# Kernel optimization log

Hardware: AMD Instinct MI355X
Metric: run time of the kernel (lower is better)

## Reference

```python
import jax, jax.numpy as jnp
import numpy as np

D, K, B, IMG, NCH = 128, 512, 8, 128, 3


def adder2d(x, w, k, stride, pad):
    # AdderNet L1 'convolution': y[b,co,l] = -sum_p |patch[b,p,l] - w[co,p]|
    # x: [B,C,H,W], w: [Cout, C*k*k]
    p = jax.lax.conv_general_dilated_patches(x, (k, k), (stride, stride), [(pad, pad), (pad, pad)])
    Bb, P, Ho, Wo = p.shape
    p = p.reshape(Bb, P, Ho * Wo)  # [B, C*k*k, L]
    def one(wc):  # wc: [P] -> [B, L]; sequential over Cout to bound memory
        return -jnp.sum(jnp.abs(p - wc[None, :, None]), axis=1)
    o = jax.lax.map(one, w)  # [Cout, B, L]
    return jnp.transpose(o, (1, 0, 2)).reshape(Bb, w.shape[0], Ho, Wo)


def bn(x, g, b, eps=1e-5):
    # eval-mode BatchNorm2d with running_mean=0, running_var=1
    s = g * jax.lax.rsqrt(jnp.asarray(1.0 + eps, x.dtype))
    return x * s[None, :, None, None] + b[None, :, None, None]


def conv2d(x, w, b, pad):
    y = jax.lax.conv_general_dilated(x, w, (1, 1), [(pad, pad), (pad, pad)],
                                     dimension_numbers=('NCHW', 'OIHW', 'NCHW'))
    return y + b[None, :, None, None]


def up2x(x):  # nn.Upsample(scale_factor=2, bilinear, align_corners=False)
    Bb, C, H, W = x.shape
    return jax.image.resize(x, (Bb, C, 2 * H, 2 * W), method='bilinear')


def adder_resblock(x, w1, w2, g, b):
    # [ReLU, adder3x3, BN, ReLU, adder1x1] + residual
    h = jax.nn.relu(x)
    h = adder2d(h, w1, 3, 1, 1)
    h = bn(h, g, b)
    h = jax.nn.relu(h)
    h = adder2d(h, w2, 1, 1, 0)
    return x + h


def conv_resblock(x, w1, b1, w2, b2):
    # [ReLU, conv3x3, ReLU, conv1x1] + residual (bn=False in decoder)
    h = jax.nn.relu(x)
    h = conv2d(h, w1, b1, 1)
    h = jax.nn.relu(h)
    h = conv2d(h, w2, b2, 0)
    return x + h


def vq_forward(z_e, E):
    # NearestEmbed: E is [d, k]
    Bb, C, H, W = z_e.shape
    flat = jnp.transpose(z_e, (0, 2, 3, 1)).reshape(-1, C)  # [N, d]
    d2 = (jnp.sum(flat * flat, axis=1, keepdims=True)
          - 2.0 * (flat @ E) + jnp.sum(E * E, axis=0)[None, :])  # [N, k]
    argmin = jnp.argmin(d2, axis=1)  # [N]
    q = jnp.take(E.T, argmin, axis=0)  # [N, d]
    # weight_sg=True path: straight-through to z_e, no grad to E
    zq_flat = flat + jax.lax.stop_gradient(q - flat)
    z_q = jnp.transpose(zq_flat.reshape(Bb, H, W, C), (0, 3, 1, 2))
    # emb path: z_e detached, grad flows to E through the gather
    emb = jnp.transpose(q.reshape(Bb, H, W, C), (0, 3, 1, 2))
    return z_q, emb, argmin.reshape(Bb, H, W)


def reference(x, we1, we2, ae1_w1, ae1_w2, ae2_w1, ae2_w2, bn_gamma, bn_beta,
              emb_weight, rd1_w1, rd1_b1, rd1_w2, rd1_b2, rd2_w1, rd2_b1,
              rd2_w2, rd2_b2, cd1_w, cd1_b, cd2_w, cd2_b):
    g, b = bn_gamma, bn_beta
    h = adder2d(x, we1, 4, 2, 1)
    h = jax.nn.relu(bn(h, g[0], b[0]))
    h = adder2d(h, we2, 4, 2, 1)
    h = jax.nn.relu(bn(h, g[1], b[1]))
    h = adder_resblock(h, ae1_w1, ae1_w2, g[2], b[2])
    h = bn(h, g[3], b[3])
    h = adder_resblock(h, ae2_w1, ae2_w2, g[4], b[4])
    z_e = bn(h, g[5], b[5])  # bne4 (gamma = 1/40)

    z_q, emb, argmin = vq_forward(z_e, emb_weight)

    y = conv_resblock(z_q, rd1_w1, rd1_b1, rd1_w2, rd1_b2)
    y = bn(y, g[6], b[6])
    y = conv_resblock(y, rd2_w1, rd2_b1, rd2_w2, rd2_b2)
    y = up2x(y)
    y = conv2d(y, cd1_w, cd1_b, 1)
    y = jax.nn.relu(bn(y, g[7], b[7]))
    y = up2x(y)
    y = conv2d(y, cd2_w, cd2_b, 1)
    y = jnp.tanh(y)
    return (y, z_e, emb, argmin)


def setup_inputs() -> dict:
    key = jax.random.key(0)
    ks = jax.random.split(key, 16)
    f = lambda k, shp: (0.02 * jax.random.normal(k, shp)).astype(jnp.float32)
    inp = {}
    inp['x'] = jax.random.normal(ks[0], (B, NCH, IMG, IMG), jnp.float32)
    inp['we1'] = f(ks[1], (D, NCH * 16))       # adder 4x4 s2
    inp['we2'] = f(ks[2], (D, D * 16))
    inp['ae1_w1'] = f(ks[3], (D, D * 9))       # adder 3x3
    inp['ae1_w2'] = f(ks[4], (D, D))           # adder 1x1
    inp['ae2_w1'] = f(ks[5], (D, D * 9))
    inp['ae2_w2'] = f(ks[6], (D, D))
    inp['bn_gamma'] = jnp.ones((8, D), jnp.float32).at[5].set(1.0 / 40.0)
    inp['bn_beta'] = jnp.zeros((8, D), jnp.float32)
    inp['emb_weight'] = f(ks[7], (D, K))
    inp['rd1_w1'] = f(ks[8], (D, D, 3, 3)); inp['rd1_b1'] = jnp.zeros(D, jnp.float32)
    inp['rd1_w2'] = f(ks[9], (D, D, 1, 1)); inp['rd1_b2'] = jnp.zeros(D, jnp.float32)
    inp['rd2_w1'] = f(ks[10], (D, D, 3, 3)); inp['rd2_b1'] = jnp.zeros(D, jnp.float32)
    inp['rd2_w2'] = f(ks[11], (D, D, 1, 1)); inp['rd2_b2'] = jnp.zeros(D, jnp.float32)
    inp['cd1_w'] = f(ks[12], (D, D, 3, 3)); inp['cd1_b'] = jnp.zeros(D, jnp.float32)
    inp['cd2_w'] = f(ks[13], (NCH, D, 3, 3)); inp['cd2_b'] = jnp.zeros(NCH, jnp.float32)
    return inp
```

## Files before the change

### kernel.cpp

```cpp
#include <hip/hip_runtime.h>
#include <math.h>

constexpr int Dc = 128;
constexpr int Kc = 512;
constexpr int Bc = 8;

template<int ISADD, int K, int STRIDE, int PAD, int IT, int EPI, int CIN, int CH,
         int PW, int OUT_ROWS, int WOUT, int WIN, int HIN, int HOUT, int COBW,
         int NW, int KSPLIT>
__global__ __launch_bounds__(NW * 64)
void lds_layer(const float* __restrict__ x, const float* __restrict__ w,
               const float* __restrict__ bias,
               const float* __restrict__ itG, const float* __restrict__ itB,
               const float* __restrict__ res,
               const float* __restrict__ rG, const float* __restrict__ rB,
               const float* __restrict__ oG, const float* __restrict__ oB,
               float* __restrict__ out) {
  constexpr int BT = NW * 64;
  constexpr int NWG = NW / KSPLIT;
  constexpr int CINW = CIN / KSPLIT;
  constexpr int CHS = KSPLIT * CH;
  constexpr int KK = K * K;
  constexpr int SPAN = (PW - 1) * STRIDE + K;
  constexpr int IN_ROWS = (OUT_ROWS - 1) * STRIDE + K;
  constexpr int WPAD = (WOUT - 1) * STRIDE + K;
  constexpr int WLDS = (WPAD + 3) & ~3;
  constexpr int PGW = WOUT / PW;
  static_assert(OUT_ROWS * PGW == 64, "one wave covers the pixel tile");
  static_assert(NW % KSPLIT == 0 && CIN % KSPLIT == 0 && CINW % CH == 0, "split");
  static_assert(KSPLIT == 1 ||
                NWG * 64 * PW * COBW <= CHS * IN_ROWS * WLDS, "scratch fits");
  constexpr int NBAND = HOUT / OUT_ROWS;
  constexpr int W4 = WIN / 4;
  constexpr int NELEM4 = CHS * IN_ROWS * W4;
  constexpr int NIT4 = (NELEM4 + BT - 1) / BT;
  constexpr bool EXACT = (NELEM4 % BT) == 0;
  const float r15 = rsqrtf(1.0f + 1e-5f);

  __shared__ alignas(16) float lds[CHS][IN_ROWS][WLDS];

  int tid = threadIdx.x;
  int gb = blockIdx.x;
  int cg = gb / (Bc * NBAND);
  int rem = gb % (Bc * NBAND);
  int band = rem % NBAND;
  int b = rem / NBAND;
  int wv = __builtin_amdgcn_readfirstlane(tid >> 6);
  int lane = tid & 63;
  int grp = wv / NWG;
  int wloc = wv % NWG;
  int co0 = cg * (NWG * COBW) + wloc * COBW;
  int pr = lane / PGW, pc = lane % PGW;
  int oh = band * OUT_ROWS + pr;
  int ow0 = pc * PW;
  int yi0 = band * OUT_ROWS * STRIDE - PAD;

  for (int e = tid; e < CHS * IN_ROWS * WLDS; e += BT) ((float*)lds)[e] = 0.f;

  float acc[PW][COBW];
#pragma unroll
  for (int p = 0; p < PW; ++p)
#pragma unroll
    for (int j = 0; j < COBW; ++j)
      acc[p][j] = (ISADD || grp != 0) ? 0.f : bias[co0 + j];

  const float* xb = x + (long)b * CIN * HIN * WIN;
  float4 rbuf[NIT4];

  auto stage = [&](int cc) {
#pragma unroll
    for (int it = 0; it < NIT4; ++it) {
      int e = it * BT + tid;
      if (!EXACT && e >= NELEM4) break;
      int c4 = e % W4;
      int r = (e / W4) % IN_ROWS;
      int ch2 = e / (W4 * IN_ROWS);
      int gc = cc + (ch2 % CH) + (ch2 / CH) * CINW;
      int yi = yi0 + r;
      float4 v = make_float4(0.f, 0.f, 0.f, 0.f);
      if (yi >= 0 && yi < HIN) {
        v = *(const float4*)&xb[((long)gc * HIN + yi) * WIN + 4 * c4];
        if (IT == 1) {
          v.x = fmaxf(v.x, 0.f); v.y = fmaxf(v.y, 0.f);
          v.z = fmaxf(v.z, 0.f); v.w = fmaxf(v.w, 0.f);
        }
        if (IT == 2) {
          float sc = itG[gc] * r15, bc = itB[gc];
          v.x = fmaxf(fmaf(v.x, sc, bc), 0.f);
          v.y = fmaxf(fmaf(v.y, sc, bc), 0.f);
          v.z = fmaxf(fmaf(v.z, sc, bc), 0.f);
          v.w = fmaxf(fmaf(v.w, sc, bc), 0.f);
        }
      }
      rbuf[it] = v;
    }
  };
  auto towrite = [&]() {
#pragma unroll
    for (int it = 0; it < NIT4; ++it) {
      int e = it * BT + tid;
      if (!EXACT && e >= NELEM4) break;
      int c4 = e % W4;
      int r = (e / W4) % IN_ROWS;
      int ch2 = e / (W4 * IN_ROWS);
      float* p = &lds[ch2][r][4 * c4 + PAD];
      float4 v = rbuf[it];
      p[0] = v.x; p[1] = v.y; p[2] = v.z; p[3] = v.w;
    }
  };

  stage(0);
  for (int cc = 0; cc < CINW; cc += CH) {
    __syncthreads();
    towrite();
    __syncthreads();
    if (cc + CH < CINW) stage(cc + CH);
#pragma unroll 2
    for (int chl = 0; chl < CH; ++chl) {
      float vbuf[K][SPAN];
#pragma unroll
      for (int kh = 0; kh < K; ++kh) {
        const float* rp0 = &lds[grp * CH + chl][pr * STRIDE + kh][ow0 * STRIDE];
        if constexpr (SPAN == 6 && (PW * STRIDE) % 4 == 0) {
          float4 a = *(const float4*)rp0;
          float2 c2 = *(const float2*)(rp0 + 4);
          vbuf[kh][0] = a.x; vbuf[kh][1] = a.y; vbuf[kh][2] = a.z;
          vbuf[kh][3] = a.w; vbuf[kh][4] = c2.x; vbuf[kh][5] = c2.y;
        } else if constexpr (SPAN == 4 && (PW * STRIDE) % 2 == 0) {
          float2 a = *(const float2*)rp0;
          float2 c2 = *(const float2*)(rp0 + 2);
          vbuf[kh][0] = a.x; vbuf[kh][1] = a.y;
          vbuf[kh][2] = c2.x; vbuf[kh][3] = c2.y;
        } else if constexpr (SPAN == 2 && (PW * STRIDE) % 2 == 0) {
          float2 a = *(const float2*)rp0;
          vbuf[kh][0] = a.x; vbuf[kh][1] = a.y;
        } else {
#pragma unroll
          for (int s = 0; s < SPAN; ++s) vbuf[kh][s] = rp0[s];
        }
      }
      const float* wc = w + ((long)co0 * CIN + (grp * CINW + cc + chl)) * KK;
#pragma unroll
      for (int kh = 0; kh < K; ++kh)
#pragma unroll
        for (int kw = 0; kw < K; ++kw)
#pragma unroll
          for (int j = 0; j < COBW; ++j) {
            float ww = wc[(long)j * CIN * KK + kh * K + kw];
#pragma unroll
            for (int p = 0; p < PW; ++p) {
              float v = vbuf[kh][p * STRIDE + kw];
              if (ISADD) acc[p][j] += fabsf(v - ww);
              else       acc[p][j] = fmaf(v, ww, acc[p][j]);
            }
          }
    }
  }

  if constexpr (KSPLIT >= 2) {
    float* scr = (float*)lds;
    int sb = (wloc * 64 + lane) * (PW * COBW);
#pragma unroll
    for (int g = 1; g < KSPLIT; ++g) {
      __syncthreads();
      if (grp == g) {
#pragma unroll
        for (int p = 0; p < PW; ++p)
#pragma unroll
          for (int j = 0; j < COBW; ++j) scr[sb + p * COBW + j] = acc[p][j];
      }
      __syncthreads();
      if (grp == 0) {
#pragma unroll
        for (int p = 0; p < PW; ++p)
#pragma unroll
          for (int j = 0; j < COBW; ++j) acc[p][j] += scr[sb + p * COBW + j];
      }
    }
    if (grp != 0) return;
  }

  long obase = ((long)(b * Dc + co0) * HOUT + oh) * WOUT + ow0;
  float* ob = out + obase;
  const float* rp = (EPI == 2 || EPI == 3 || EPI == 6) ? res + obase : nullptr;
  constexpr long hw = (long)HOUT * WOUT;
#pragma unroll
  for (int j = 0; j < COBW; ++j) {
    float og = 0.f, obb = 0.f, rg = 0.f, rbb = 0.f;
    if (EPI == 1 || EPI == 6) { og = oG[co0 + j] * r15; obb = oB[co0 + j]; }
    if (EPI == 3 || EPI == 6) { rg = rG[co0 + j] * r15; rbb = rB[co0 + j]; }
#pragma unroll
    for (int p = 0; p < PW; ++p) {
      float val = ISADD ? -acc[p][j] : acc[p][j];
      if (EPI == 1) val = fmaxf(fmaf(val, og, obb), 0.f);
      if (EPI == 2) val = rp[j * hw + p] + val;
      if (EPI == 3) val = fmaf(rp[j * hw + p], rg, rbb) + val;
      if (EPI == 5) val = fmaxf(val, 0.f);
      if (EPI == 6) val = fmaf(fmaf(rp[j * hw + p], rg, rbb) + val, og, obb);
      ob[j * hw + p] = val;
    }
  }
}

template<int ISADD, int EPI, int COBW>
__global__ __launch_bounds__(256)
void pw1x1(const float* __restrict__ x, const float* __restrict__ w,
           const float* __restrict__ bias,
           const float* __restrict__ res,
           const float* __restrict__ rG, const float* __restrict__ rB,
           const float* __restrict__ oG, const float* __restrict__ oB,
           float* __restrict__ out) {
  constexpr int HW = 1024;
  constexpr int CIN = Dc;
  constexpr int KS = 4;
  constexpr int CSEG = CIN / KS;
  constexpr int PXB = 128;
  constexpr int NPG = HW / PXB;
  constexpr int OPT = (PXB * COBW) / 256;
  static_assert(OPT * 256 == PXB * COBW, "combine exact");
  const float r15 = rsqrtf(1.0f + 1e-5f);

  __shared__ float scr[KS][COBW][PXB];

  int tid = threadIdx.x;
  int wv = __builtin_amdgcn_readfirstlane(tid >> 6);
  int lane = tid & 63;
  int gb = blockIdx.x;
  int cg = gb / (Bc * NPG);
  int rem = gb % (Bc * NPG);
  int pg = rem % NPG;
  int b = rem / NPG;
  int co0 = cg * COBW;
  int px = pg * PXB + lane * 2;

  const float* xc = x + ((long)b * CIN + wv * CSEG) * HW + px;
  const float* wseg = w + wv * CSEG;

  float acc[2][COBW];
#pragma unroll
  for (int p = 0; p < 2; ++p)
#pragma unroll
    for (int j = 0; j < COBW; ++j) acc[p][j] = 0.f;

#pragma unroll 4
  for (int c = 0; c < CSEG; ++c) {
    float2 v = *(const float2*)&xc[(long)c * HW];
#pragma unroll
    for (int j = 0; j < COBW; ++j) {
      float ww = wseg[(long)(co0 + j) * CIN + c];
      if (ISADD) {
        acc[0][j] += fabsf(v.x - ww);
        acc[1][j] += fabsf(v.y - ww);
      } else {
        acc[0][j] = fmaf(v.x, ww, acc[0][j]);
        acc[1][j] = fmaf(v.y, ww, acc[1][j]);
      }
    }
  }

#pragma unroll
  for (int j = 0; j < COBW; ++j) {
    float2 t = make_float2(acc[0][j], acc[1][j]);
    *(float2*)&scr[wv][j][lane * 2] = t;
  }
  __syncthreads();

#pragma unroll
  for (int k = 0; k < OPT; ++k) {
    int e = k * 256 + tid;
    int pxl = e % PXB;
    int j = e / PXB;
    float s = scr[0][j][pxl] + scr[1][j][pxl] + scr[2][j][pxl] + scr[3][j][pxl];
    float val = ISADD ? -s : s + bias[co0 + j];
    long oidx = ((long)b * Dc + co0 + j) * HW + pg * PXB + pxl;
    if (EPI == 2) val = res[oidx] + val;
    if (EPI == 3) {
      float rg = rG[co0 + j] * r15, rbb = rB[co0 + j];
      val = fmaf(res[oidx], rg, rbb) + val;
    }
    if (EPI == 6) {
      float rg = rG[co0 + j] * r15, rbb = rB[co0 + j];
      float og = oG[co0 + j] * r15, obb = oB[co0 + j];
      val = fmaf(fmaf(res[oidx], rg, rbb) + val, og, obb);
    }
    out[oidx] = val;
  }
}

__device__ __forceinline__ void up_coef(int p, int H, int& i0, int& i1, float& w0, float& w1) {
  int m = p >> 1;
  if ((p & 1) == 0) { i0 = (m > 0) ? m - 1 : 0; i1 = m; w0 = 0.25f; w1 = 0.75f; }
  else              { i0 = m; i1 = (m + 1 < H) ? m + 1 : H - 1; w0 = 0.75f; w1 = 0.25f; }
}

__global__ void up2x_kernel(const float* __restrict__ in, float* __restrict__ out,
                            int C, int H, int W) {
  int H2 = 2 * H, W2 = 2 * W;
  int i = blockIdx.x * blockDim.x + threadIdx.x;
  int total = Bc * C * H2 * W2;
  if (i >= total) return;
  int ow = i % W2; int t = i / W2;
  int oh = t % H2; t /= H2;
  int c = t % C; int b = t / C;
  int y0, y1, x0, x1; float wy0, wy1, wx0, wx1;
  up_coef(oh, H, y0, y1, wy0, wy1);
  up_coef(ow, W, x0, x1, wx0, wx1);
  const float* p = in + (b * C + c) * H * W;
  float v = wy0 * (wx0 * p[y0 * W + x0] + wx1 * p[y0 * W + x1])
          + wy1 * (wx0 * p[y1 * W + x0] + wx1 * p[y1 * W + x1]);
  out[i] = v;
}

__global__ __launch_bounds__(256)
void conv3x3_up_tanh_ks(const float* __restrict__ x, const float* __restrict__ w,
                        const float* __restrict__ bias, float* __restrict__ out,
                        int Hs, int Ws, int Cout) {
  constexpr int CIN = Dc;
  constexpr int SEG = 4;
  constexpr int CSEG = CIN / SEG;
  constexpr int QB = 64;
  __shared__ float scr[SEG][4][QB];

  int H2 = 2 * Hs, W2 = 2 * Ws;
  int nq = Hs * Ws;
  int tid = threadIdx.x;
  int q_l = tid % QB;
  int seg = tid / QB;
  int gq = blockIdx.x * QB + q_l;
  int q = gq % nq; int t2 = gq / nq;
  int co = t2 % Cout; int b = t2 / Cout;
  int n = q % Ws, m = q / Ws;
  int rows[3] = { (m > 0) ? m - 1 : 0, m, (m + 1 < Hs) ? m + 1 : Hs - 1 };
  int cols[3] = { (n > 0) ? n - 1 : 0, n, (n + 1 < Ws) ? n + 1 : Ws - 1 };
  float rv[4] = { (2 * m - 1 >= 0) ? 1.f : 0.f, 1.f, 1.f, (2 * m + 2 < H2) ? 1.f : 0.f };
  float cv[4] = { (2 * n - 1 >= 0) ? 1.f : 0.f, 1.f, 1.f, (2 * n + 2 < W2) ? 1.f : 0.f };
  float acc[4] = { 0.f, 0.f, 0.f, 0.f };
  const float* xb = x + (b * CIN + seg * CSEG) * nq;
  const float* wb = w + (co * CIN + seg * CSEG) * 9;
  for (int c = 0; c < CSEG; ++c) {
    const float* xc = xb + c * nq;
    float s[3][3];
#pragma unroll
    for (int a = 0; a < 3; ++a)
#pragma unroll
      for (int e = 0; e < 3; ++e) s[a][e] = xc[rows[a] * Ws + cols[e]];
    float rb[4][3];
#pragma unroll
    for (int e = 0; e < 3; ++e) {
      rb[0][e] = fmaf(0.75f, s[0][e], 0.25f * s[1][e]);
      rb[1][e] = fmaf(0.25f, s[0][e], 0.75f * s[1][e]);
      rb[2][e] = fmaf(0.75f, s[1][e], 0.25f * s[2][e]);
      rb[3][e] = fmaf(0.25f, s[1][e], 0.75f * s[2][e]);
    }
    float u[4][4];
#pragma unroll
    for (int di = 0; di < 4; ++di) {
      float rm = rv[di];
      u[di][0] = fmaf(0.75f, rb[di][0], 0.25f * rb[di][1]) * rm * cv[0];
      u[di][1] = fmaf(0.25f, rb[di][0], 0.75f * rb[di][1]) * rm * cv[1];
      u[di][2] = fmaf(0.75f, rb[di][1], 0.25f * rb[di][2]) * rm * cv[2];
      u[di][3] = fmaf(0.25f, rb[di][1], 0.75f * rb[di][2]) * rm * cv[3];
    }
    const float* wc = wb + c * 9;
#pragma unroll
    for (int kh = 0; kh < 3; ++kh)
#pragma unroll
      for (int kw = 0; kw < 3; ++kw) {
        float ww = wc[kh * 3 + kw];
        acc[0] = fmaf(u[kh][kw],         ww, acc[0]);
        acc[1] = fmaf(u[kh][kw + 1],     ww, acc[1]);
        acc[2] = fmaf(u[kh + 1][kw],     ww, acc[2]);
        acc[3] = fmaf(u[kh + 1][kw + 1], ww, acc[3]);
      }
  }
#pragma unroll
  for (int di = 0; di < 4; ++di) scr[seg][di][q_l] = acc[di];
  __syncthreads();
  int di = tid / QB;
  float sum = scr[0][di][q_l] + scr[1][di][q_l] + scr[2][di][q_l]
            + scr[3][di][q_l] + bias[co];
  out[(long)(b * Cout + co) * H2 * W2 + (2 * m + (di >> 1)) * W2 + 2 * n + (di & 1)]
      = tanhf(sum);
}

__global__ __launch_bounds__(256)
void vq_kernel8(const float* __restrict__ z_e, const float* __restrict__ E,
                float* __restrict__ emb, float* __restrict__ argmin_out) {
  constexpr int HW = 1024;
  __shared__ alignas(16) float f[8][Dc];
  __shared__ float d2s[8][256];
  __shared__ int   ks[8][256];
  int tid = threadIdx.x;
  int n0 = blockIdx.x * 8;
  int b = n0 >> 10;
  int rem = n0 & 1023;
  const float* zb = z_e + (long)b * Dc * HW + rem;
#pragma unroll
  for (int i = 0; i < 4; ++i) {
    int e = i * 256 + tid;
    int p = e & 7, d = e >> 3;
    f[p][d] = zb[d * HW + p];
  }
  __syncthreads();
  float f2 = 0.f;
  if (tid < 8) {
    for (int d = 0; d < Dc; ++d) f2 += f[tid][d] * f[tid][d];
    d2s[tid][0] = f2;
  }
  __syncthreads();
  float f2v[8];
#pragma unroll
  for (int p = 0; p < 8; ++p) f2v[p] = d2s[p][0];
  __syncthreads();

  float best[8]; int bk[8];
#pragma unroll
  for (int p = 0; p < 8; ++p) { best[p] = 3.4e38f; bk[p] = 0; }
  for (int kk = tid; kk < Kc; kk += 256) {
    float dot[8];
#pragma unroll
    for (int p = 0; p < 8; ++p) dot[p] = 0.f;
    float e2k = 0.f;
    for (int d4 = 0; d4 < Dc; d4 += 4) {
      float e0 = E[(long)(d4 + 0) * Kc + kk];
      float e1 = E[(long)(d4 + 1) * Kc + kk];
      float e2c = E[(long)(d4 + 2) * Kc + kk];
      float e3 = E[(long)(d4 + 3) * Kc + kk];
      e2k = fmaf(e0, e0, e2k);
      e2k = fmaf(e1, e1, e2k);
      e2k = fmaf(e2c, e2c, e2k);
      e2k = fmaf(e3, e3, e2k);
#pragma unroll
      for (int p = 0; p < 8; ++p) {
        float4 fv = *(const float4*)&f[p][d4];
        dot[p] = fmaf(fv.x, e0, dot[p]);
        dot[p] = fmaf(fv.y, e1, dot[p]);
        dot[p] = fmaf(fv.z, e2c, dot[p]);
        dot[p] = fmaf(fv.w, e3, dot[p]);
      }
    }
#pragma unroll
    for (int p = 0; p < 8; ++p) {
      float d2 = f2v[p] - 2.f * dot[p] + e2k;
      if (d2 < best[p] || (d2 == best[p] && kk < bk[p])) { best[p] = d2; bk[p] = kk; }
    }
  }
#pragma unroll
  for (int p = 0; p < 8; ++p) { d2s[p][tid] = best[p]; ks[p][tid] = bk[p]; }
  __syncthreads();
  for (int s = 128; s > 0; s >>= 1) {
    if (tid < s) {
#pragma unroll
      for (int p = 0; p < 8; ++p) {
        float ob = d2s[p][tid + s]; int ok = ks[p][tid + s];
        if (ob < d2s[p][tid] || (ob == d2s[p][tid] && ok < ks[p][tid])) {
          d2s[p][tid] = ob; ks[p][tid] = ok;
        }
      }
    }
    __syncthreads();
  }
  if (tid < 8) argmin_out[n0 + tid] = (float)ks[tid][0];
  float* eb = emb + (long)b * Dc * HW + rem;
#pragma unroll
  for (int i = 0; i < 4; ++i) {
    int e = i * 256 + tid;
    int p = e & 7, d = e >> 3;
    eb[d * HW + p] = E[d * Kc + ks[p][0]];
  }
}

extern "C" void kernel_launch(void* const* d_in, const int* in_sizes, int n_in,
                              void* d_out, int out_size, void* d_ws, size_t ws_size,
                              hipStream_t stream) {
  const float* x      = (const float*)d_in[0];
  const float* we1    = (const float*)d_in[1];
  const float* we2    = (const float*)d_in[2];
  const float* ae1_w1 = (const float*)d_in[3];
  const float* ae1_w2 = (const float*)d_in[4];
  const float* ae2_w1 = (const float*)d_in[5];
  const float* ae2_w2 = (const float*)d_in[6];
  const float* bn_g   = (const float*)d_in[7];
  const float* bn_b   = (const float*)d_in[8];
  const float* embw   = (const float*)d_in[9];
  const float* rd1_w1 = (const float*)d_in[10];
  const float* rd1_b1 = (const float*)d_in[11];
  const float* rd1_w2 = (const float*)d_in[12];
  const float* rd1_b2 = (const float*)d_in[13];
  const float* rd2_w1 = (const float*)d_in[14];
  const float* rd2_b1 = (const float*)d_in[15];
  const float* rd2_w2 = (const float*)d_in[16];
  const float* rd2_b2 = (const float*)d_in[17];
  const float* cd1_w  = (const float*)d_in[18];
  const float* cd1_b  = (const float*)d_in[19];
  const float* cd2_w  = (const float*)d_in[20];
  const float* cd2_b  = (const float*)d_in[21];

  const float* g0 = bn_g + 0 * Dc; const float* b0 = bn_b + 0 * Dc;
  const float* g1 = bn_g + 1 * Dc; const float* b1 = bn_b + 1 * Dc;
  const float* g2 = bn_g + 2 * Dc; const float* b2 = bn_b + 2 * Dc;
  const float* g3 = bn_g + 3 * Dc; const float* b3 = bn_b + 3 * Dc;
  const float* g4 = bn_g + 4 * Dc; const float* b4 = bn_b + 4 * Dc;
  const float* g5 = bn_g + 5 * Dc; const float* b5 = bn_b + 5 * Dc;
  const float* g6 = bn_g + 6 * Dc; const float* b6 = bn_b + 6 * Dc;
  const float* g7 = bn_g + 7 * Dc; const float* b7 = bn_b + 7 * Dc;

  float* W64a = (float*)d_ws;
  float* W64b = W64a + 4194304;
  float* Wa   = W64b + 4194304;
  float* Wb   = Wa + 1048576;
  float* Wc   = Wb + 1048576;

  float* out_y   = (float*)d_out;
  float* out_ze  = out_y  + 393216;
  float* out_emb = out_ze + 1048576;
  float* out_am  = out_emb + 1048576;

  const int TB = 256;
  const int TB8 = 512;
  auto nb = [](int n) { return (n + 255) / 256; };
  const int N64 = Bc * Dc * 64 * 64;
  const float* nul = nullptr;

  const int G32s = 16 * Bc * 8;
  const int Gwe1 = 8 * Bc * 32;
  const int Gcd1 = 4 * Bc * 32;
  const int Gpw  = 32 * Bc * 8;
  const int Gct  = Bc * 3 * 64 * 64 / 64;

  lds_layer<1,4,2,1, 0,1, 3,3, 2, 2,64,128,128,64, 4,4,1><<<Gwe1, TB, 0, stream>>>(
      x, we1, nul, nul, nul, nul, nul, nul, g0, b0, W64a);
  lds_layer<1,4,2,1, 0,1, Dc,4, 2, 4,32,64,64,32, 2,8,2><<<G32s, TB8, 0, stream>>>(
      W64a, we2, nul, nul, nul, nul, nul, nul, g1, b1, Wa);
  lds_layer<1,3,1,1, 0,1, Dc,16, 2, 4,32,32,32,32, 2,8,2><<<G32s, TB8, 0, stream>>>(
      Wa, ae1_w1, nul, nul, nul, nul, nul, nul, g2, b2, Wb);
  pw1x1<1,2,4><<<Gpw, TB, 0, stream>>>(
      Wb, ae1_w2, nul, Wa, nul, nul, nul, nul, Wc);
  lds_layer<1,3,1,1, 2,1, Dc,16, 2, 4,32,32,32,32, 2,8,2><<<G32s, TB8, 0, stream>>>(
      Wc, ae2_w1, nul, g3, b3, nul, nul, nul, g4, b4, Wb);
  pw1x1<1,6,4><<<Gpw, TB, 0, stream>>>(
      Wb, ae2_w2, nul, Wc, g3, b3, g5, b5, out_ze);

  vq_kernel8<<<Bc * 1024 / 8, 256, 0, stream>>>(out_ze, embw, out_emb, out_am);

  lds_layer<0,3,1,1, 1,5, Dc,16, 2, 4,32,32,32,32, 2,8,2><<<G32s, TB8, 0, stream>>>(
      out_emb, rd1_w1, rd1_b1, nul, nul, nul, nul, nul, nul, nul, Wb);
  pw1x1<0,2,4><<<Gpw, TB, 0, stream>>>(
      Wb, rd1_w2, rd1_b2, out_emb, nul, nul, nul, nul, Wa);
  lds_layer<0,3,1,1, 2,5, Dc,16, 2, 4,32,32,32,32, 2,8,2><<<G32s, TB8, 0, stream>>>(
      Wa, rd2_w1, rd2_b1, g6, b6, nul, nul, nul, nul, nul, Wb);
  pw1x1<0,3,4><<<Gpw, TB, 0, stream>>>(
      Wb, rd2_w2, rd2_b2, Wa, g6, b6, nul, nul, Wc);

  up2x_kernel<<<nb(N64), TB, 0, stream>>>(Wc, W64a, Dc, 32, 32);
  lds_layer<0,3,1,1, 0,1, Dc,8, 2, 2,64,64,64,64, 8,8,2><<<Gcd1, TB8, 0, stream>>>(
      W64a, cd1_w, cd1_b, nul, nul, nul, nul, nul, g7, b7, W64b);

  conv3x3_up_tanh_ks<<<Gct, TB, 0, stream>>>(W64b, cd2_w, cd2_b, out_y, 64, 64, 3);
}
```

Baseline: 783.7 us.

## Vectorize upsample to two outputs per thread, widen VQ and tanh-conv parallelism

The bilinear upsample kernel now has each thread compute two horizontally adjacent outputs from a shared three-column row blend and store them as a float2, which cuts redundant loads and index math. The VQ kernel moves to 512 threads so each thread handles exactly one codebook entry with no inner loop, and the argmin reduction gains one more level. The final upsample+conv+tanh kernel splits the channel reduction into 8 segments over 32 query points per block instead of 4 over 64, doubling the grid. These are three separate parallelism and vectorization tweaks to small kernels, each trading extra blocks or reduction steps for shorter per-thread work.

```diff
diff --git a/kernel.cpp b/kernel.cpp
--- a/kernel.cpp
+++ b/kernel.cpp
@@ -293,22 +293,25 @@
   else              { i0 = m; i1 = (m + 1 < H) ? m + 1 : H - 1; w0 = 0.75f; w1 = 0.25f; }
 }
 
-__global__ void up2x_kernel(const float* __restrict__ in, float* __restrict__ out,
-                            int C, int H, int W) {
+__global__ void up2x2_kernel(const float* __restrict__ in, float* __restrict__ out,
+                             int C, int H, int W) {
   int H2 = 2 * H, W2 = 2 * W;
   int i = blockIdx.x * blockDim.x + threadIdx.x;
-  int total = Bc * C * H2 * W2;
+  int total = Bc * C * H2 * W;
   if (i >= total) return;
-  int ow = i % W2; int t = i / W2;
-  int oh = t % H2; t /= H2;
-  int c = t % C; int b = t / C;
-  int y0, y1, x0, x1; float wy0, wy1, wx0, wx1;
+  int t = i % W; int u = i / W;
+  int oh = u % H2; u /= H2;
+  int c = u % C; int b = u / C;
+  int y0, y1; float wy0, wy1;
   up_coef(oh, H, y0, y1, wy0, wy1);
-  up_coef(ow, W, x0, x1, wx0, wx1);
   const float* p = in + (b * C + c) * H * W;
-  float v = wy0 * (wx0 * p[y0 * W + x0] + wx1 * p[y0 * W + x1])
-          + wy1 * (wx0 * p[y1 * W + x0] + wx1 * p[y1 * W + x1]);
-  out[i] = v;
+  int xm1 = (t > 0) ? t - 1 : 0;
+  int xp1 = (t + 1 < W) ? t + 1 : W - 1;
+  float r0 = wy0 * p[y0 * W + xm1] + wy1 * p[y1 * W + xm1];
+  float r1 = wy0 * p[y0 * W + t]   + wy1 * p[y1 * W + t];
+  float r2 = wy0 * p[y0 * W + xp1] + wy1 * p[y1 * W + xp1];
+  float2 o = make_float2(0.25f * r0 + 0.75f * r1, 0.75f * r1 + 0.25f * r2);
+  *(float2*)&out[((long)(b * C + c) * H2 + oh) * W2 + 2 * t] = o;
 }
 
 __global__ __launch_bounds__(256)
@@ -316,9 +319,9 @@
                         const float* __restrict__ bias, float* __restrict__ out,
                         int Hs, int Ws, int Cout) {
   constexpr int CIN = Dc;
-  constexpr int SEG = 4;
+  constexpr int SEG = 8;
   constexpr int CSEG = CIN / SEG;
-  constexpr int QB = 64;
+  constexpr int QB = 32;
   __shared__ float scr[SEG][4][QB];
 
   int H2 = 2 * Hs, W2 = 2 * Ws;
@@ -376,28 +379,36 @@
 #pragma unroll
   for (int di = 0; di < 4; ++di) scr[seg][di][q_l] = acc[di];
   __syncthreads();
-  int di = tid / QB;
-  float sum = scr[0][di][q_l] + scr[1][di][q_l] + scr[2][di][q_l]
-            + scr[3][di][q_l] + bias[co];
-  out[(long)(b * Cout + co) * H2 * W2 + (2 * m + (di >> 1)) * W2 + 2 * n + (di & 1)]
-      = tanhf(sum);
-}
-
-__global__ __launch_bounds__(256)
+  if (tid < 4 * QB) {
+    int ql2 = tid % QB;
+    int di = tid / QB;
+    int gq2 = blockIdx.x * QB + ql2;
+    int q2 = gq2 % nq; int t3 = gq2 / nq;
+    int co2 = t3 % Cout; int b2 = t3 / Cout;
+    int n2 = q2 % Ws, m2 = q2 / Ws;
+    float sum = bias[co2];
+#pragma unroll
+    for (int sg = 0; sg < SEG; ++sg) sum += scr[sg][di][ql2];
+    out[(long)(b2 * Cout + co2) * H2 * W2 + (2 * m2 + (di >> 1)) * W2 + 2 * n2 + (di & 1)]
+        = tanhf(sum);
+  }
+}
+
+__global__ __launch_bounds__(512)
 void vq_kernel8(const float* __restrict__ z_e, const float* __restrict__ E,
                 float* __restrict__ emb, float* __restrict__ argmin_out) {
   constexpr int HW = 1024;
   __shared__ alignas(16) float f[8][Dc];
-  __shared__ float d2s[8][256];
-  __shared__ int   ks[8][256];
+  __shared__ float d2s[8][512];
+  __shared__ int   ks[8][512];
   int tid = threadIdx.x;
   int n0 = blockIdx.x * 8;
   int b = n0 >> 10;
   int rem = n0 & 1023;
   const float* zb = z_e + (long)b * Dc * HW + rem;
 #pragma unroll
-  for (int i = 0; i < 4; ++i) {
-    int e = i * 256 + tid;
+  for (int i = 0; i < 2; ++i) {
+    int e = i * 512 + tid;
     int p = e & 7, d = e >> 3;
     f[p][d] = zb[d * HW + p];
   }
@@ -413,42 +424,36 @@
   for (int p = 0; p < 8; ++p) f2v[p] = d2s[p][0];
   __syncthreads();
 
-  float best[8]; int bk[8];
-#pragma unroll
-  for (int p = 0; p < 8; ++p) { best[p] = 3.4e38f; bk[p] = 0; }
-  for (int kk = tid; kk < Kc; kk += 256) {
-    float dot[8];
-#pragma unroll
-    for (int p = 0; p < 8; ++p) dot[p] = 0.f;
-    float e2k = 0.f;
-    for (int d4 = 0; d4 < Dc; d4 += 4) {
-      float e0 = E[(long)(d4 + 0) * Kc + kk];
-      float e1 = E[(long)(d4 + 1) * Kc + kk];
-      float e2c = E[(long)(d4 + 2) * Kc + kk];
-      float e3 = E[(long)(d4 + 3) * Kc + kk];
-      e2k = fmaf(e0, e0, e2k);
-      e2k = fmaf(e1, e1, e2k);
-      e2k = fmaf(e2c, e2c, e2k);
-      e2k = fmaf(e3, e3, e2k);
-#pragma unroll
-      for (int p = 0; p < 8; ++p) {
-        float4 fv = *(const float4*)&f[p][d4];
-        dot[p] = fmaf(fv.x, e0, dot[p]);
-        dot[p] = fmaf(fv.y, e1, dot[p]);
-        dot[p] = fmaf(fv.z, e2c, dot[p]);
-        dot[p] = fmaf(fv.w, e3, dot[p]);
-      }
-    }
+  int kk = tid;
+  float dot[8];
+#pragma unroll
+  for (int p = 0; p < 8; ++p) dot[p] = 0.f;
+  float e2k = 0.f;
+  for (int d4 = 0; d4 < Dc; d4 += 4) {
+    float e0 = E[(long)(d4 + 0) * Kc + kk];
+    float e1 = E[(long)(d4 + 1) * Kc + kk];
+    float e2c = E[(long)(d4 + 2) * Kc + kk];
+    float e3 = E[(long)(d4 + 3) * Kc + kk];
+    e2k = fmaf(e0, e0, e2k);
+    e2k = fmaf(e1, e1, e2k);
+    e2k = fmaf(e2c, e2c, e2k);
+    e2k = fmaf(e3, e3, e2k);
 #pragma unroll
     for (int p = 0; p < 8; ++p) {
-      float d2 = f2v[p] - 2.f * dot[p] + e2k;
-      if (d2 < best[p] || (d2 == best[p] && kk < bk[p])) { best[p] = d2; bk[p] = kk; }
-    }
-  }
-#pragma unroll
-  for (int p = 0; p < 8; ++p) { d2s[p][tid] = best[p]; ks[p][tid] = bk[p]; }
+      float4 fv = *(const float4*)&f[p][d4];
+      dot[p] = fmaf(fv.x, e0, dot[p]);
+      dot[p] = fmaf(fv.y, e1, dot[p]);
+      dot[p] = fmaf(fv.z, e2c, dot[p]);
+      dot[p] = fmaf(fv.w, e3, dot[p]);
+    }
+  }
+#pragma unroll
+  for (int p = 0; p < 8; ++p) {
+    d2s[p][tid] = f2v[p] - 2.f * dot[p] + e2k;
+    ks[p][tid] = kk;
+  }
   __syncthreads();
-  for (int s = 128; s > 0; s >>= 1) {
+  for (int s = 256; s > 0; s >>= 1) {
     if (tid < s) {
 #pragma unroll
       for (int p = 0; p < 8; ++p) {
@@ -463,8 +468,8 @@
   if (tid < 8) argmin_out[n0 + tid] = (float)ks[tid][0];
   float* eb = emb + (long)b * Dc * HW + rem;
 #pragma unroll
-  for (int i = 0; i < 4; ++i) {
-    int e = i * 256 + tid;
+  for (int i = 0; i < 2; ++i) {
+    int e = i * 512 + tid;
     int p = e & 7, d = e >> 3;
     eb[d * HW + p] = E[d * Kc + ks[p][0]];
   }
@@ -519,14 +524,14 @@
   const int TB = 256;
   const int TB8 = 512;
   auto nb = [](int n) { return (n + 255) / 256; };
-  const int N64 = Bc * Dc * 64 * 64;
   const float* nul = nullptr;
 
   const int G32s = 16 * Bc * 8;
   const int Gwe1 = 8 * Bc * 32;
   const int Gcd1 = 4 * Bc * 32;
   const int Gpw  = 32 * Bc * 8;
-  const int Gct  = Bc * 3 * 64 * 64 / 64;
+  const int Gct  = Bc * 3 * 64 * 64 / 32;
+  const int Gup  = nb(Bc * Dc * 64 * 32);
 
   lds_layer<1,4,2,1, 0,1, 3,3, 2, 2,64,128,128,64, 4,4,1><<<Gwe1, TB, 0, stream>>>(
       x, we1, nul, nul, nul, nul, nul, nul, g0, b0, W64a);
@@ -541,7 +546,7 @@
   pw1x1<1,6,4><<<Gpw, TB, 0, stream>>>(
       Wb, ae2_w2, nul, Wc, g3, b3, g5, b5, out_ze);
 
-  vq_kernel8<<<Bc * 1024 / 8, 256, 0, stream>>>(out_ze, embw, out_emb, out_am);
+  vq_kernel8<<<Bc * 1024 / 8, 512, 0, stream>>>(out_ze, embw, out_emb, out_am);
 
   lds_layer<0,3,1,1, 1,5, Dc,16, 2, 4,32,32,32,32, 2,8,2><<<G32s, TB8, 0, stream>>>(
       out_emb, rd1_w1, rd1_b1, nul, nul, nul, nul, nul, nul, nul, Wb);
@@ -552,7 +557,7 @@
   pw1x1<0,3,4><<<Gpw, TB, 0, stream>>>(
       Wb, rd2_w2, rd2_b2, Wa, g6, b6, nul, nul, Wc);
 
-  up2x_kernel<<<nb(N64), TB, 0, stream>>>(Wc, W64a, Dc, 32, 32);
+  up2x2_kernel<<<Gup, TB, 0, stream>>>(Wc, W64a, Dc, 32, 32);
   lds_layer<0,3,1,1, 0,1, Dc,8, 2, 2,64,64,64,64, 8,8,2><<<Gcd1, TB8, 0, stream>>>(
       W64a, cd1_w, cd1_b, nul, nul, nul, nul, nul, g7, b7, W64b);
 
```

Result: no change. 781.5 us (median of 2 runs) (-0.3%).
